# Performance work log

Hardware: AMD Instinct MI355X
Metric: run time of the kernel (lower is better)

The kernel has to match this reference:

```python
import jax, jax.numpy as jnp
import numpy as np

DIM = 1024
HIDDEN = 4096
NUM_EXPERTS = 8
TOP_K = 2
T = 8192


def setup_inputs() -> dict:
    key = jax.random.key(0)
    ks = jax.random.split(key, 5)
    scale = 0.02
    x = jax.random.normal(ks[0], (T, DIM), dtype=jnp.float32)
    gate_w = jax.random.normal(ks[1], (NUM_EXPERTS, DIM), dtype=jnp.float32) * scale  # Linear weight [out,in]
    w1 = jax.random.normal(ks[2], (NUM_EXPERTS, HIDDEN, DIM), dtype=jnp.float32) * scale
    w2 = jax.random.normal(ks[3], (NUM_EXPERTS, DIM, HIDDEN), dtype=jnp.float32) * scale
    w3 = jax.random.normal(ks[4], (NUM_EXPERTS, HIDDEN, DIM), dtype=jnp.float32) * scale
    return {"x": x, "gate_w": gate_w, "w1": w1, "w2": w2, "w3": w3}


def reference(x, gate_w, w1, w2, w3):
    # Router: softmax over all experts, take top-2, renormalize.
    logits = jnp.einsum('td,ed->te', x, gate_w)            # [T, E]
    probs = jax.nn.softmax(logits, axis=-1)
    topw, topi = jax.lax.top_k(probs, TOP_K)               # [T, 2]
    topw = topw / jnp.sum(topw, axis=-1, keepdims=True)
    out = jnp.zeros_like(x)
    num_experts = w1.shape[0]
    for e in range(num_experts):
        # combine weight for expert e per token (0 if not routed here)
        w_e = jnp.sum(jnp.where(topi == e, topw, 0.0), axis=-1)   # [T]
        h = jax.nn.silu(x @ w1[e].T) * (x @ w3[e].T)              # [T, HIDDEN]
        out = out + w_e[:, None] * (h @ w2[e].T)                  # [T, DIM]
    return out
```

## Files before the change

kernel.cpp:

```cpp
#include <hip/hip_runtime.h>
#include <hip/hip_bf16.h>
#include <cstdint>
#include <cstddef>

#define TK 8192
#define DIM 1024
#define HID 4096
#define NE 8

#define BMT 256
#define BNT 256
#define BKT 32
#define NBUF 4

typedef __attribute__((ext_vector_type(8))) __bf16 bfrag;
typedef __attribute__((ext_vector_type(4))) float ffrag;

static __device__ __forceinline__ ushort f2bf(float f) {
    union { float f; uint32_t u; } v; v.f = f;
    uint32_t r = (v.u + 0x7fffu + ((v.u >> 16) & 1u)) >> 16;
    return (ushort)r;
}

static __device__ __forceinline__ uint4 pack8(float4 a, float4 b) {
    union { ushort u[8]; uint4 q; } pk;
    pk.u[0] = f2bf(a.x); pk.u[1] = f2bf(a.y); pk.u[2] = f2bf(a.z); pk.u[3] = f2bf(a.w);
    pk.u[4] = f2bf(b.x); pk.u[5] = f2bf(b.y); pk.u[6] = f2bf(b.z); pk.u[7] = f2bf(b.w);
    return pk.q;
}

static __device__ __forceinline__ void gld16(const ushort* g, ushort* l) {
    __builtin_amdgcn_global_load_lds(
        (const __attribute__((address_space(1))) unsigned int*)g,
        (__attribute__((address_space(3))) unsigned int*)l, 16, 0, 0);
}

#define BARRIER() asm volatile("s_barrier" ::: "memory")
#define WAITVM(N) asm volatile("s_waitcnt vmcnt(" #N ")" ::: "memory")

#define LDSIDX(r, kc) ((((r) >> 3) << 8) + ((kc) << 6) + (((r) & 7) << 3))
#define SLOT_R(s)  ((((s) >> 5) << 3) | ((s) & 7))
#define SLOT_KC(s) (((s) >> 3) & 3)

__global__ __launch_bounds__(256) void k_cvt(const float* __restrict__ src,
                                             ushort* __restrict__ dst, int n8) {
    int i = blockIdx.x * blockDim.x + threadIdx.x;
    if (i >= n8) return;
    const float4* p = (const float4*)src + (size_t)i * 2;
    ((uint4*)dst)[i] = pack8(p[0], p[1]);
}

__global__ __launch_bounds__(256) void k_router(const float* __restrict__ x,
                                                const float* __restrict__ gw,
                                                int* __restrict__ topi, float* __restrict__ topw) {
    int t = blockIdx.x * 4 + (threadIdx.x >> 6);
    int lane = threadIdx.x & 63;
    if (t >= TK) return;
    double acc[NE];
#pragma unroll
    for (int e = 0; e < NE; ++e) acc[e] = 0.0;
    const float* xr = x + (size_t)t * DIM;
    for (int k = lane; k < DIM; k += 64) {
        double xv = (double)xr[k];
#pragma unroll
        for (int e = 0; e < NE; ++e) acc[e] += xv * (double)gw[e * DIM + k];
    }
#pragma unroll
    for (int e = 0; e < NE; ++e) {
#pragma unroll
        for (int off = 32; off > 0; off >>= 1) acc[e] += __shfl_xor(acc[e], off);
    }
    if (lane == 0) {
        int i1 = 0;
#pragma unroll
        for (int e = 1; e < NE; ++e) if (acc[e] > acc[i1]) i1 = e;
        int i2 = (i1 == 0) ? 1 : 0;
#pragma unroll
        for (int e = 0; e < NE; ++e) if (e != i1 && acc[e] > acc[i2]) i2 = e;
        double w = 1.0 / (1.0 + exp(acc[i2] - acc[i1]));
        topi[t * 2 + 0] = i1; topi[t * 2 + 1] = i2;
        topw[t * 2 + 0] = (float)w; topw[t * 2 + 1] = (float)(1.0 - w);
    }
}

__global__ void k_count(const int* __restrict__ topi, int* __restrict__ counts) {
    int i = blockIdx.x * blockDim.x + threadIdx.x;
    if (i < 2 * TK) atomicAdd(&counts[topi[i]], 1);
}

__global__ void k_scan(const int* __restrict__ counts, int* __restrict__ offs, int* __restrict__ cursor) {
    if (threadIdx.x == 0 && blockIdx.x == 0) {
        int s = 0;
        for (int e = 0; e < NE; ++e) { offs[e] = s; cursor[e] = s; s += counts[e]; }
        offs[NE] = s;
    }
}

__global__ void k_scatter(const int* __restrict__ topi, const float* __restrict__ topw,
                          int* __restrict__ cursor, int* __restrict__ perm, float* __restrict__ pw) {
    int t = blockIdx.x * blockDim.x + threadIdx.x;
    if (t >= TK) return;
#pragma unroll
    for (int k = 0; k < 2; ++k) {
        int e = topi[t * 2 + k];
        int pos = atomicAdd(&cursor[e], 1);
        perm[pos] = t; pw[pos] = topw[t * 2 + k];
    }
}

__global__ __launch_bounds__(512, 2) void k_ffn1(const ushort* __restrict__ xb,
                                                 const ushort* __restrict__ w1b,
                                                 const ushort* __restrict__ w3b,
                                                 const int* __restrict__ offs,
                                                 const int* __restrict__ perm,
                                                 ushort* __restrict__ H) {
    const int g = blockIdx.x;
    const int xcd = g & 7, kk = g >> 3;
    const int p  = xcd + ((kk >> 5) << 3);
    const int mt = kk & 31;
    const int e  = p >> 5, nt = p & 31;

    const int off = offs[e], end = offs[e + 1];
    const int m0 = off + mt * BMT;
    if (m0 >= end) return;
    const int nrows = min(BMT, end - m0);

    __shared__ ushort lA[NBUF][BMT * BKT];
    __shared__ ushort lB[NBUF][BNT * BKT];
    __shared__ int lTok[BMT];

    const int tid = threadIdx.x;
    if (tid < BMT) lTok[tid] = (tid < nrows) ? perm[m0 + tid] : -1;
    __syncthreads();

    const int lane = tid & 63, wid = tid >> 6;
    const int wm = (wid >> 2) * 128;
    const int wn = (wid & 3) * 64;

    ffrag acc[8][4];
#pragma unroll
    for (int i = 0; i < 8; ++i)
#pragma unroll
        for (int j = 0; j < 4; ++j) acc[i][j] = (ffrag)0.f;

    const ushort* pA[2]; const ushort* pB[2];
    {
        const size_t ebase = (size_t)e * HID * DIM;
#pragma unroll
        for (int i = 0; i < 2; ++i) {
            int s = i * 512 + tid;
            int r = SLOT_R(s), kc = SLOT_KC(s);
            int tok = lTok[r]; if (tok < 0) tok = 0;
            pA[i] = xb + (size_t)tok * DIM + kc * 8;
            int gg = r >> 4;
            int h  = ((gg >> 1) << 4) | (r & 15);
            const ushort* wsrc = (gg & 1) ? w3b : w1b;
            pB[i] = wsrc + ebase + (size_t)(nt * 128 + h) * DIM + kc * 8;
        }
    }

#define STG1A(buf, k0) do { \
        gld16(pA[0] + (k0), &lA[buf][(wid * 64) * 8]); \
        gld16(pA[1] + (k0), &lA[buf][(512 + wid * 64) * 8]); } while (0)
#define STG1B(buf, k0) do { \
        gld16(pB[0] + (k0), &lB[buf][(wid * 64) * 8]); \
        gld16(pB[1] + (k0), &lB[buf][(512 + wid * 64) * 8]); } while (0)

    STG1A(0, 0);  STG1B(0, 0);
    STG1A(1, 32); STG1B(1, 32);
    STG1A(2, 64); STG1B(2, 64);

    const int NT = DIM / BKT;
#pragma unroll 1
    for (int t = 0; t < NT; ++t) {
        const int cbuf = t & 3, sbuf = (t + 3) & 3;
        const bool stg = (t + 3) < NT;
        const int sk0 = (t + 3) * BKT;
        if (t + 2 < NT) { WAITVM(8); } else if (t + 1 < NT) { WAITVM(4); } else { WAITVM(0); }
        BARRIER();
        if (stg) STG1A(sbuf, sk0);
        const int kcc = lane >> 4;
        bfrag a[8], b[4];
#pragma unroll
        for (int j = 0; j < 4; ++j)
            b[j] = *(const bfrag*)&lB[cbuf][LDSIDX(wn + j * 16 + (lane & 15), kcc)];
#pragma unroll
        for (int i = 0; i < 4; ++i)
            a[i] = *(const bfrag*)&lA[cbuf][LDSIDX(wm + i * 16 + (lane & 15), kcc)];
        __builtin_amdgcn_s_setprio(1);
#pragma unroll
        for (int i = 0; i < 4; ++i)
#pragma unroll
            for (int j = 0; j < 4; ++j)
                acc[i][j] = __builtin_amdgcn_mfma_f32_16x16x32_bf16(a[i], b[j], acc[i][j], 0, 0, 0);
        __builtin_amdgcn_s_setprio(0);
        if (stg) STG1B(sbuf, sk0);
#pragma unroll
        for (int i = 4; i < 8; ++i)
            a[i] = *(const bfrag*)&lA[cbuf][LDSIDX(wm + i * 16 + (lane & 15), kcc)];
        __builtin_amdgcn_s_setprio(1);
#pragma unroll
        for (int i = 4; i < 8; ++i)
#pragma unroll
            for (int j = 0; j < 4; ++j)
                acc[i][j] = __builtin_amdgcn_mfma_f32_16x16x32_bf16(a[i], b[j], acc[i][j], 0, 0, 0);
        __builtin_amdgcn_s_setprio(0);
    }
#undef STG1A
#undef STG1B

#pragma unroll
    for (int i = 0; i < 8; ++i) {
        int rbase = wm + i * 16 + ((lane >> 4) << 2);
#pragma unroll
        for (int q = 0; q < 4; ++q) {
            int rl = rbase + q;
            if (rl >= nrows) continue;
            size_t rowoff = (size_t)(m0 + rl) * HID;
#pragma unroll
            for (int jf = 0; jf < 4; jf += 2) {
                int gg = (wn >> 4) + jf;
                int col = nt * 128 + ((gg >> 1) << 4) + (lane & 15);
                float h1 = acc[i][jf][q], h3 = acc[i][jf + 1][q];
                float val = (h1 / (1.f + __expf(-h1))) * h3;
                H[rowoff + col] = f2bf(val);
            }
        }
    }
}

__global__ __launch_bounds__(512, 2) void k_ffn2(const ushort* __restrict__ H,
                                                 const ushort* __restrict__ w2b,
                                                 const int* __restrict__ offs,
                                                 const int* __restrict__ perm,
                                                 const float* __restrict__ pw,
                                                 float* __restrict__ out) {
    const int g = blockIdx.x;
    const int xcd = g & 7, kk = g >> 3;
    const int p  = xcd + ((kk >> 5) << 3);
    const int mt = kk & 31;
    const int e  = p >> 2, nt = p & 3;

    const int off = offs[e], end = offs[e + 1];
    const int m0 = off + mt * BMT;
    if (m0 >= end) return;
    const int nrows = min(BMT, end - m0);

    __shared__ ushort lA[NBUF][BMT * BKT];
    __shared__ ushort lB[NBUF][BNT * BKT];
    __shared__ int lTok[BMT];
    __shared__ float lPw[BMT];

    const int tid = threadIdx.x;
    if (tid < BMT) {
        bool v = tid < nrows;
        lTok[tid] = v ? perm[m0 + tid] : -1;
        lPw[tid]  = v ? pw[m0 + tid] : 0.f;
    }
    __syncthreads();

    const int lane = tid & 63, wid = tid >> 6;
    const int wm = (wid >> 2) * 128;
    const int wn = (wid & 3) * 64;

    ffrag acc[8][4];
#pragma unroll
    for (int i = 0; i < 8; ++i)
#pragma unroll
        for (int j = 0; j < 4; ++j) acc[i][j] = (ffrag)0.f;

    const ushort* pA[2]; const ushort* pB[2];
    {
        const size_t ebase = (size_t)e * DIM * HID;
#pragma unroll
        for (int i = 0; i < 2; ++i) {
            int s = i * 512 + tid;
            int r = SLOT_R(s), kc = SLOT_KC(s);
            int pos = m0 + r; if (pos > 2 * TK - 1) pos = 2 * TK - 1;
            pA[i] = H + (size_t)pos * HID + kc * 8;
            pB[i] = w2b + ebase + (size_t)(nt * BNT + r) * HID + kc * 8;
        }
    }

#define STG2A(buf, k0) do { \
        gld16(pA[0] + (k0), &lA[buf][(wid * 64) * 8]); \
        gld16(pA[1] + (k0), &lA[buf][(512 + wid * 64) * 8]); } while (0)
#define STG2B(buf, k0) do { \
        gld16(pB[0] + (k0), &lB[buf][(wid * 64) * 8]); \
        gld16(pB[1] + (k0), &lB[buf][(512 + wid * 64) * 8]); } while (0)

    STG2A(0, 0);  STG2B(0, 0);
    STG2A(1, 32); STG2B(1, 32);
    STG2A(2, 64); STG2B(2, 64);

    const int NT = HID / BKT;
#pragma unroll 1
    for (int t = 0; t < NT; ++t) {
        const int cbuf = t & 3, sbuf = (t + 3) & 3;
        const bool stg = (t + 3) < NT;
        const int sk0 = (t + 3) * BKT;
        if (t + 2 < NT) { WAITVM(8); } else if (t + 1 < NT) { WAITVM(4); } else { WAITVM(0); }
        BARRIER();
        if (stg) STG2A(sbuf, sk0);
        const int kcc = lane >> 4;
        bfrag a[8], b[4];
#pragma unroll
        for (int j = 0; j < 4; ++j)
            b[j] = *(const bfrag*)&lB[cbuf][LDSIDX(wn + j * 16 + (lane & 15), kcc)];
#pragma unroll
        for (int i = 0; i < 4; ++i)
            a[i] = *(const bfrag*)&lA[cbuf][LDSIDX(wm + i * 16 + (lane & 15), kcc)];
        __builtin_amdgcn_s_setprio(1);
#pragma unroll
        for (int i = 0; i < 4; ++i)
#pragma unroll
            for (int j = 0; j < 4; ++j)
                acc[i][j] = __builtin_amdgcn_mfma_f32_16x16x32_bf16(a[i], b[j], acc[i][j], 0, 0, 0);
        __builtin_amdgcn_s_setprio(0);
        if (stg) STG2B(sbuf, sk0);
#pragma unroll
        for (int i = 4; i < 8; ++i)
            a[i] = *(const bfrag*)&lA[cbuf][LDSIDX(wm + i * 16 + (lane & 15), kcc)];
        __builtin_amdgcn_s_setprio(1);
#pragma unroll
        for (int i = 4; i < 8; ++i)
#pragma unroll
            for (int j = 0; j < 4; ++j)
                acc[i][j] = __builtin_amdgcn_mfma_f32_16x16x32_bf16(a[i], b[j], acc[i][j], 0, 0, 0);
        __builtin_amdgcn_s_setprio(0);
    }
#undef STG2A
#undef STG2B

    const int colbase = nt * BNT + wn;
#pragma unroll
    for (int i = 0; i < 8; ++i) {
        int rbase = wm + i * 16 + ((lane >> 4) << 2);
#pragma unroll
        for (int q = 0; q < 4; ++q) {
            int rl = rbase + q;
            if (rl >= nrows) continue;
            int tok = lTok[rl];
            float w = lPw[rl];
            if (tok < 0) continue;
            size_t rowoff = (size_t)tok * DIM;
#pragma unroll
            for (int j = 0; j < 4; ++j) {
                int col = colbase + j * 16 + (lane & 15);
                atomicAdd(&out[rowoff + col], acc[i][j][q] * w);
            }
        }
    }
}

extern "C" void kernel_launch(void* const* d_in, const int* in_sizes, int n_in,
                              void* d_out, int out_size, void* d_ws, size_t ws_size,
                              hipStream_t stream) {
    const float* x  = (const float*)d_in[0];
    const float* gw = (const float*)d_in[1];
    const float* w1 = (const float*)d_in[2];
    const float* w2 = (const float*)d_in[3];
    const float* w3 = (const float*)d_in[4];
    float* out = (float*)d_out;

    char* ws = (char*)d_ws;
    int*    topi   = (int*)(ws + 0);
    float*  topw   = (float*)(ws + 65536);
    int*    perm   = (int*)(ws + 131072);
    float*  pw     = (float*)(ws + 196608);
    int*    counts = (int*)(ws + 262144);
    int*    offs   = (int*)(ws + 262144 + 256);
    int*    cursor = (int*)(ws + 262144 + 512);

    const size_t OFF_XB = 524288;
    const size_t OFF_H  = OFF_XB + 16777216;
    const size_t OFF_WA = OFF_H + 134217728;
    const size_t OFF_WB = OFF_WA + 67108864;

    ushort* xb  = (ushort*)(ws + OFF_XB);
    ushort* H   = (ushort*)(ws + OFF_H);
    ushort* wA  = (ushort*)(ws + OFF_WA);
    ushort* wB  = (ushort*)(ws + OFF_WB);

    hipMemsetAsync(counts, 0, 32, stream);
    hipMemsetAsync(out, 0, (size_t)out_size * sizeof(float), stream);

    k_router<<<dim3(TK / 4), 256, 0, stream>>>(x, gw, topi, topw);
    k_count<<<dim3((2 * TK) / 256), 256, 0, stream>>>(topi, counts);
    k_scan<<<dim3(1), 64, 0, stream>>>(counts, offs, cursor);
    k_scatter<<<dim3(TK / 256), 256, 0, stream>>>(topi, topw, cursor, perm, pw);

    k_cvt<<<dim3((TK * DIM / 8) / 256), 256, 0, stream>>>(x, xb, TK * DIM / 8);
    k_cvt<<<dim3((NE * HID * DIM / 8) / 256), 256, 0, stream>>>(w1, wA, NE * HID * DIM / 8);
    k_cvt<<<dim3((NE * HID * DIM / 8) / 256), 256, 0, stream>>>(w3, wB, NE * HID * DIM / 8);

    k_ffn1<<<dim3(8192), 512, 0, stream>>>(xb, wA, wB, offs, perm, H);

    k_cvt<<<dim3((NE * DIM * HID / 8) / 256), 256, 0, stream>>>(w2, wA, NE * DIM * HID / 8);

    k_ffn2<<<dim3(1024), 512, 0, stream>>>(H, wA, offs, perm, pw, out);
}
```

Baseline: 1.202 ms.

## Restructure GEMM main loops into unrolled half-tile phases and regroup FFN2 block mapping

Both FFN GEMM loops are rewritten as a manually unrolled sequence of eight phases per four K-steps. Each phase loads half the A fragments, issues one stage of global-to-LDS prefetch, waits and barriers, then runs 16 MFMAs, in a ping-pong style schedule that keeps fewer A fragments in registers. In k_ffn2 the block-index mapping is changed so the four N-tiles of one M-tile land together on the same XCD, which should improve L2 reuse of the H rows. The extra barriers per phase add synchronization overhead and the waitcnt logic becomes less precise, which risks stalls or correctness issues near the end of the loop.

```diff
diff --git a/kernel.cpp b/kernel.cpp
--- a/kernel.cpp
+++ b/kernel.cpp
@@ -10,7 +10,7 @@
 
 #define BMT 256
 #define BNT 256
-#define BKT 32
+#define SK 32
 #define NBUF 4
 
 typedef __attribute__((ext_vector_type(8))) __bf16 bfrag;
@@ -107,6 +107,7 @@
         perm[pos] = t; pw[pos] = topw[t * 2 + k];
     }
 }
+
 
 __global__ __launch_bounds__(512, 2) void k_ffn1(const ushort* __restrict__ xb,
                                                  const ushort* __restrict__ w1b,
@@ -125,8 +126,8 @@
     if (m0 >= end) return;
     const int nrows = min(BMT, end - m0);
 
-    __shared__ ushort lA[NBUF][BMT * BKT];
-    __shared__ ushort lB[NBUF][BNT * BKT];
+    __shared__ ushort lA[NBUF][BMT * SK];
+    __shared__ ushort lB[NBUF][BNT * SK];
     __shared__ int lTok[BMT];
 
     const int tid = threadIdx.x;
@@ -134,6 +135,7 @@
     __syncthreads();
 
     const int lane = tid & 63, wid = tid >> 6;
+    const int l15 = lane & 15;
     const int wm = (wid >> 2) * 128;
     const int wn = (wid & 3) * 64;
 
@@ -159,55 +161,60 @@
         }
     }
 
-#define STG1A(buf, k0) do { \
-        gld16(pA[0] + (k0), &lA[buf][(wid * 64) * 8]); \
-        gld16(pA[1] + (k0), &lA[buf][(512 + wid * 64) * 8]); } while (0)
-#define STG1B(buf, k0) do { \
-        gld16(pB[0] + (k0), &lB[buf][(wid * 64) * 8]); \
-        gld16(pB[1] + (k0), &lB[buf][(512 + wid * 64) * 8]); } while (0)
-
-    STG1A(0, 0);  STG1B(0, 0);
-    STG1A(1, 32); STG1B(1, 32);
-    STG1A(2, 64); STG1B(2, 64);
-
-    const int NT = DIM / BKT;
+    const int NSUB = DIM / SK;
+
+#define STGA(buf, sx) do { if ((sx) < NSUB) { \
+        gld16(pA[0] + (sx) * SK, &lA[buf][(wid * 64) * 8]); \
+        gld16(pA[1] + (sx) * SK, &lA[buf][(512 + wid * 64) * 8]); } } while (0)
+#define STGB(buf, sx) do { if ((sx) < NSUB) { \
+        gld16(pB[0] + (sx) * SK, &lB[buf][(wid * 64) * 8]); \
+        gld16(pB[1] + (sx) * SK, &lB[buf][(512 + wid * 64) * 8]); } } while (0)
+
+    bfrag a[4], b[4];
+#define PH(buf, IH, STG) do {                                                   \
+        const int kcc = lane >> 4;                                              \
+        if (IH == 0) {                                                          \
+            _Pragma("unroll")                                                   \
+            for (int j = 0; j < 4; ++j)                                         \
+                b[j] = *(const bfrag*)&lB[buf][LDSIDX(wn + j * 16 + l15, kcc)]; \
+        }                                                                       \
+        _Pragma("unroll")                                                       \
+        for (int i = 0; i < 4; ++i)                                             \
+            a[i] = *(const bfrag*)&lA[buf][LDSIDX(wm + IH * 64 + i * 16 + l15, kcc)]; \
+        STG;                                                                    \
+        WAITVM(8); BARRIER();                                                   \
+        __builtin_amdgcn_s_setprio(1);                                          \
+        _Pragma("unroll")                                                       \
+        for (int i = 0; i < 4; ++i)                                             \
+            _Pragma("unroll")                                                   \
+            for (int j = 0; j < 4; ++j)                                         \
+                acc[IH * 4 + i][j] = __builtin_amdgcn_mfma_f32_16x16x32_bf16(a[i], b[j], acc[IH * 4 + i][j], 0, 0, 0); \
+        __builtin_amdgcn_s_setprio(0);                                          \
+        BARRIER();                                                              \
+    } while (0)
+
+    STGA(0, 0); STGB(0, 0);
+    STGA(1, 1); STGB(1, 1);
+    STGA(2, 2); STGB(2, 2);
+    WAITVM(8);
+    BARRIER();
+
 #pragma unroll 1
-    for (int t = 0; t < NT; ++t) {
-        const int cbuf = t & 3, sbuf = (t + 3) & 3;
-        const bool stg = (t + 3) < NT;
-        const int sk0 = (t + 3) * BKT;
-        if (t + 2 < NT) { WAITVM(8); } else if (t + 1 < NT) { WAITVM(4); } else { WAITVM(0); }
-        BARRIER();
-        if (stg) STG1A(sbuf, sk0);
-        const int kcc = lane >> 4;
-        bfrag a[8], b[4];
-#pragma unroll
-        for (int j = 0; j < 4; ++j)
-            b[j] = *(const bfrag*)&lB[cbuf][LDSIDX(wn + j * 16 + (lane & 15), kcc)];
-#pragma unroll
-        for (int i = 0; i < 4; ++i)
-            a[i] = *(const bfrag*)&lA[cbuf][LDSIDX(wm + i * 16 + (lane & 15), kcc)];
-        __builtin_amdgcn_s_setprio(1);
-#pragma unroll
-        for (int i = 0; i < 4; ++i)
-#pragma unroll
-            for (int j = 0; j < 4; ++j)
-                acc[i][j] = __builtin_amdgcn_mfma_f32_16x16x32_bf16(a[i], b[j], acc[i][j], 0, 0, 0);
-        __builtin_amdgcn_s_setprio(0);
-        if (stg) STG1B(sbuf, sk0);
-#pragma unroll
-        for (int i = 4; i < 8; ++i)
-            a[i] = *(const bfrag*)&lA[cbuf][LDSIDX(wm + i * 16 + (lane & 15), kcc)];
-        __builtin_amdgcn_s_setprio(1);
-#pragma unroll
-        for (int i = 4; i < 8; ++i)
-#pragma unroll
-            for (int j = 0; j < 4; ++j)
-                acc[i][j] = __builtin_amdgcn_mfma_f32_16x16x32_bf16(a[i], b[j], acc[i][j], 0, 0, 0);
-        __builtin_amdgcn_s_setprio(0);
-    }
-#undef STG1A
-#undef STG1B
+    for (int m = 0; m < NSUB / 4; ++m) {
+        const int s3 = 4 * m + 3, s4 = 4 * m + 4, s5 = 4 * m + 5, s6 = 4 * m + 6;
+        PH(0, 0, STGA(3, s3));
+        PH(0, 1, STGB(3, s3));
+        PH(1, 0, STGA(0, s4));
+        PH(1, 1, STGB(0, s4));
+        PH(2, 0, STGA(1, s5));
+        PH(2, 1, STGB(1, s5));
+        PH(3, 0, STGA(2, s6));
+        PH(3, 1, STGB(2, s6));
+    }
+    WAITVM(0);
+#undef PH
+#undef STGA
+#undef STGB
 
 #pragma unroll
     for (int i = 0; i < 8; ++i) {
@@ -220,7 +227,7 @@
 #pragma unroll
             for (int jf = 0; jf < 4; jf += 2) {
                 int gg = (wn >> 4) + jf;
-                int col = nt * 128 + ((gg >> 1) << 4) + (lane & 15);
+                int col = nt * 128 + ((gg >> 1) << 4) + l15;
                 float h1 = acc[i][jf][q], h3 = acc[i][jf + 1][q];
                 float val = (h1 / (1.f + __expf(-h1))) * h3;
                 H[rowoff + col] = f2bf(val);
@@ -236,18 +243,18 @@
                                                  const float* __restrict__ pw,
                                                  float* __restrict__ out) {
     const int g = blockIdx.x;
-    const int xcd = g & 7, kk = g >> 3;
-    const int p  = xcd + ((kk >> 5) << 3);
-    const int mt = kk & 31;
-    const int e  = p >> 2, nt = p & 3;
+    const int xcd = g & 7, k = g >> 3;
+    const int gg = xcd + ((k >> 2) << 3);
+    const int nt = k & 3;
+    const int e = gg >> 5, mt = gg & 31;
 
     const int off = offs[e], end = offs[e + 1];
     const int m0 = off + mt * BMT;
     if (m0 >= end) return;
     const int nrows = min(BMT, end - m0);
 
-    __shared__ ushort lA[NBUF][BMT * BKT];
-    __shared__ ushort lB[NBUF][BNT * BKT];
+    __shared__ ushort lA[NBUF][BMT * SK];
+    __shared__ ushort lB[NBUF][BNT * SK];
     __shared__ int lTok[BMT];
     __shared__ float lPw[BMT];
 
@@ -260,6 +267,7 @@
     __syncthreads();
 
     const int lane = tid & 63, wid = tid >> 6;
+    const int l15 = lane & 15;
     const int wm = (wid >> 2) * 128;
     const int wn = (wid & 3) * 64;
 
@@ -282,55 +290,60 @@
         }
     }
 
-#define STG2A(buf, k0) do { \
-        gld16(pA[0] + (k0), &lA[buf][(wid * 64) * 8]); \
-        gld16(pA[1] + (k0), &lA[buf][(512 + wid * 64) * 8]); } while (0)
-#define STG2B(buf, k0) do { \
-        gld16(pB[0] + (k0), &lB[buf][(wid * 64) * 8]); \
-        gld16(pB[1] + (k0), &lB[buf][(512 + wid * 64) * 8]); } while (0)
-
-    STG2A(0, 0);  STG2B(0, 0);
-    STG2A(1, 32); STG2B(1, 32);
-    STG2A(2, 64); STG2B(2, 64);
-
-    const int NT = HID / BKT;
+    const int NSUB = HID / SK;
+
+#define STGA(buf, sx) do { if ((sx) < NSUB) { \
+        gld16(pA[0] + (sx) * SK, &lA[buf][(wid * 64) * 8]); \
+        gld16(pA[1] + (sx) * SK, &lA[buf][(512 + wid * 64) * 8]); } } while (0)
+#define STGB(buf, sx) do { if ((sx) < NSUB) { \
+        gld16(pB[0] + (sx) * SK, &lB[buf][(wid * 64) * 8]); \
+        gld16(pB[1] + (sx) * SK, &lB[buf][(512 + wid * 64) * 8]); } } while (0)
+
+    bfrag a[4], b[4];
+#define PH(buf, IH, STG) do {                                                   \
+        const int kcc = lane >> 4;                                              \
+        if (IH == 0) {                                                          \
+            _Pragma("unroll")                                                   \
+            for (int j = 0; j < 4; ++j)                                         \
+                b[j] = *(const bfrag*)&lB[buf][LDSIDX(wn + j * 16 + l15, kcc)]; \
+        }                                                                       \
+        _Pragma("unroll")                                                       \
+        for (int i = 0; i < 4; ++i)                                             \
+            a[i] = *(const bfrag*)&lA[buf][LDSIDX(wm + IH * 64 + i * 16 + l15, kcc)]; \
+        STG;                                                                    \
+        WAITVM(8); BARRIER();                                                   \
+        __builtin_amdgcn_s_setprio(1);                                          \
+        _Pragma("unroll")                                                       \
+        for (int i = 0; i < 4; ++i)                                             \
+            _Pragma("unroll")                                                   \
+            for (int j = 0; j < 4; ++j)                                         \
+                acc[IH * 4 + i][j] = __builtin_amdgcn_mfma_f32_16x16x32_bf16(a[i], b[j], acc[IH * 4 + i][j], 0, 0, 0); \
+        __builtin_amdgcn_s_setprio(0);                                          \
+        BARRIER();                                                              \
+    } while (0)
+
+    STGA(0, 0); STGB(0, 0);
+    STGA(1, 1); STGB(1, 1);
+    STGA(2, 2); STGB(2, 2);
+    WAITVM(8);
+    BARRIER();
+
 #pragma unroll 1
-    for (int t = 0; t < NT; ++t) {
-        const int cbuf = t & 3, sbuf = (t + 3) & 3;
-        const bool stg = (t + 3) < NT;
-        const int sk0 = (t + 3) * BKT;
-        if (t + 2 < NT) { WAITVM(8); } else if (t + 1 < NT) { WAITVM(4); } else { WAITVM(0); }
-        BARRIER();
-        if (stg) STG2A(sbuf, sk0);
-        const int kcc = lane >> 4;
-        bfrag a[8], b[4];
-#pragma unroll
-        for (int j = 0; j < 4; ++j)
-            b[j] = *(const bfrag*)&lB[cbuf][LDSIDX(wn + j * 16 + (lane & 15), kcc)];
-#pragma unroll
-        for (int i = 0; i < 4; ++i)
-            a[i] = *(const bfrag*)&lA[cbuf][LDSIDX(wm + i * 16 + (lane & 15), kcc)];
-        __builtin_amdgcn_s_setprio(1);
-#pragma unroll
-        for (int i = 0; i < 4; ++i)
-#pragma unroll
-            for (int j = 0; j < 4; ++j)
-                acc[i][j] = __builtin_amdgcn_mfma_f32_16x16x32_bf16(a[i], b[j], acc[i][j], 0, 0, 0);
-        __builtin_amdgcn_s_setprio(0);
-        if (stg) STG2B(sbuf, sk0);
-#pragma unroll
-        for (int i = 4; i < 8; ++i)
-            a[i] = *(const bfrag*)&lA[cbuf][LDSIDX(wm + i * 16 + (lane & 15), kcc)];
-        __builtin_amdgcn_s_setprio(1);
-#pragma unroll
-        for (int i = 4; i < 8; ++i)
-#pragma unroll
-            for (int j = 0; j < 4; ++j)
-                acc[i][j] = __builtin_amdgcn_mfma_f32_16x16x32_bf16(a[i], b[j], acc[i][j], 0, 0, 0);
-        __builtin_amdgcn_s_setprio(0);
-    }
-#undef STG2A
-#undef STG2B
+    for (int m = 0; m < NSUB / 4; ++m) {
+        const int s3 = 4 * m + 3, s4 = 4 * m + 4, s5 = 4 * m + 5, s6 = 4 * m + 6;
+        PH(0, 0, STGA(3, s3));
+        PH(0, 1, STGB(3, s3));
+        PH(1, 0, STGA(0, s4));
+        PH(1, 1, STGB(0, s4));
+        PH(2, 0, STGA(1, s5));
+        PH(2, 1, STGB(1, s5));
+        PH(3, 0, STGA(2, s6));
+        PH(3, 1, STGB(2, s6));
+    }
+    WAITVM(0);
+#undef PH
+#undef STGA
+#undef STGB
 
     const int colbase = nt * BNT + wn;
 #pragma unroll
@@ -346,7 +359,7 @@
             size_t rowoff = (size_t)tok * DIM;
 #pragma unroll
             for (int j = 0; j < 4; ++j) {
-                int col = colbase + j * 16 + (lane & 15);
+                int col = colbase + j * 16 + l15;
                 atomicAdd(&out[rowoff + col], acc[i][j][q] * w);
             }
         }
```

New measurement: 1.021 ms. 15.1% less time.

## Persistent grouped-GEMM kernels with compact tile descriptors and smaller M tiles

Applied to the files above, without the earlier changes.

The scan kernel now builds a compact list of (expert, m-tile) descriptors, and both FFN kernels become persistent grid-stride loops over only the valid work items. Before, most of the 8192 launched blocks exited early. M tiles shrink from 256 to 128 rows, the pipeline drops from 4 buffers to 3, and launch bounds rise to 4 blocks per CU to raise occupancy and cut the padding waste from partial tiles. In exchange, each 128-row tile now reloads its full weight slice, so total weight traffic doubles, and the XCD-aware block remapping is gone, which may hurt L2 locality.

```diff
diff --git a/kernel.cpp b/kernel.cpp
--- a/kernel.cpp
+++ b/kernel.cpp
@@ -8,10 +8,11 @@
 #define HID 4096
 #define NE 8
 
-#define BMT 256
-#define BNT 256
-#define BKT 32
-#define NBUF 4
+#define SK 32
+#define NSUB1 (DIM / SK)
+#define NSUB2 (HID / SK)
+#define ASZ (512 * 8)
+#define BSZ (1024 * 8)
 
 typedef __attribute__((ext_vector_type(8))) __bf16 bfrag;
 typedef __attribute__((ext_vector_type(4))) float ffrag;
@@ -88,11 +89,19 @@
     if (i < 2 * TK) atomicAdd(&counts[topi[i]], 1);
 }
 
-__global__ void k_scan(const int* __restrict__ counts, int* __restrict__ offs, int* __restrict__ cursor) {
+__global__ void k_scan(const int* __restrict__ counts, int* __restrict__ offs,
+                       int* __restrict__ cursor, int* __restrict__ desc,
+                       int* __restrict__ ndesc) {
     if (threadIdx.x == 0 && blockIdx.x == 0) {
-        int s = 0;
-        for (int e = 0; e < NE; ++e) { offs[e] = s; cursor[e] = s; s += counts[e]; }
+        int s = 0, d = 0;
+        for (int e = 0; e < NE; ++e) {
+            offs[e] = s; cursor[e] = s;
+            int tiles = (counts[e] + 127) >> 7;
+            for (int t = 0; t < tiles; ++t) desc[d++] = (e << 16) | t;
+            s += counts[e];
+        }
         offs[NE] = s;
+        ndesc[0] = d;
     }
 }
 
@@ -108,246 +117,251 @@
     }
 }
 
-__global__ __launch_bounds__(512, 2) void k_ffn1(const ushort* __restrict__ xb,
+
+__global__ __launch_bounds__(512, 4) void k_ffn1(const ushort* __restrict__ xb,
                                                  const ushort* __restrict__ w1b,
                                                  const ushort* __restrict__ w3b,
                                                  const int* __restrict__ offs,
                                                  const int* __restrict__ perm,
+                                                 const int* __restrict__ desc,
+                                                 const int* __restrict__ ndesc_g,
                                                  ushort* __restrict__ H) {
-    const int g = blockIdx.x;
-    const int xcd = g & 7, kk = g >> 3;
-    const int p  = xcd + ((kk >> 5) << 3);
-    const int mt = kk & 31;
-    const int e  = p >> 5, nt = p & 31;
-
-    const int off = offs[e], end = offs[e + 1];
-    const int m0 = off + mt * BMT;
-    if (m0 >= end) return;
-    const int nrows = min(BMT, end - m0);
-
-    __shared__ ushort lA[NBUF][BMT * BKT];
-    __shared__ ushort lB[NBUF][BNT * BKT];
-    __shared__ int lTok[BMT];
+    __shared__ ushort lA[3 * ASZ];
+    __shared__ ushort lB[3 * BSZ];
+    __shared__ int lTok[128];
 
     const int tid = threadIdx.x;
-    if (tid < BMT) lTok[tid] = (tid < nrows) ? perm[m0 + tid] : -1;
-    __syncthreads();
-
     const int lane = tid & 63, wid = tid >> 6;
-    const int wm = (wid >> 2) * 128;
+    const int l15 = lane & 15, kcc = lane >> 4;
+    const int wm = (wid >> 2) * 64;
     const int wn = (wid & 3) * 64;
 
-    ffrag acc[8][4];
-#pragma unroll
-    for (int i = 0; i < 8; ++i)
-#pragma unroll
-        for (int j = 0; j < 4; ++j) acc[i][j] = (ffrag)0.f;
-
-    const ushort* pA[2]; const ushort* pB[2];
-    {
-        const size_t ebase = (size_t)e * HID * DIM;
-#pragma unroll
-        for (int i = 0; i < 2; ++i) {
-            int s = i * 512 + tid;
-            int r = SLOT_R(s), kc = SLOT_KC(s);
-            int tok = lTok[r]; if (tok < 0) tok = 0;
-            pA[i] = xb + (size_t)tok * DIM + kc * 8;
-            int gg = r >> 4;
-            int h  = ((gg >> 1) << 4) | (r & 15);
-            const ushort* wsrc = (gg & 1) ? w3b : w1b;
-            pB[i] = wsrc + ebase + (size_t)(nt * 128 + h) * DIM + kc * 8;
-        }
-    }
-
-#define STG1A(buf, k0) do { \
-        gld16(pA[0] + (k0), &lA[buf][(wid * 64) * 8]); \
-        gld16(pA[1] + (k0), &lA[buf][(512 + wid * 64) * 8]); } while (0)
-#define STG1B(buf, k0) do { \
-        gld16(pB[0] + (k0), &lB[buf][(wid * 64) * 8]); \
-        gld16(pB[1] + (k0), &lB[buf][(512 + wid * 64) * 8]); } while (0)
-
-    STG1A(0, 0);  STG1B(0, 0);
-    STG1A(1, 32); STG1B(1, 32);
-    STG1A(2, 64); STG1B(2, 64);
-
-    const int NT = DIM / BKT;
+    const int nitems = ndesc_g[0] << 5;
+
+    const int rA = SLOT_R(tid), kcA = SLOT_KC(tid);
+
+    bfrag a[4], b[4];
+    ffrag acc[4][4];
+
 #pragma unroll 1
-    for (int t = 0; t < NT; ++t) {
-        const int cbuf = t & 3, sbuf = (t + 3) & 3;
-        const bool stg = (t + 3) < NT;
-        const int sk0 = (t + 3) * BKT;
-        if (t + 2 < NT) { WAITVM(8); } else if (t + 1 < NT) { WAITVM(4); } else { WAITVM(0); }
-        BARRIER();
-        if (stg) STG1A(sbuf, sk0);
-        const int kcc = lane >> 4;
-        bfrag a[8], b[4];
-#pragma unroll
-        for (int j = 0; j < 4; ++j)
-            b[j] = *(const bfrag*)&lB[cbuf][LDSIDX(wn + j * 16 + (lane & 15), kcc)];
+    for (int w = blockIdx.x; w < nitems; w += (int)gridDim.x) {
+        __syncthreads();
+        const int de = desc[w >> 5];
+        const int e = de >> 16, mt = de & 0xffff, nt = w & 31;
+        const int m0 = offs[e] + (mt << 7);
+        const int nrows = min(128, offs[e + 1] - m0);
+        if (tid < 128) lTok[tid] = (tid < nrows) ? perm[m0 + tid] : perm[m0];
+        __syncthreads();
+
+        const ushort* pA = xb + (size_t)lTok[rA] * DIM + kcA * 8;
+        const ushort* pBp[2];
+        {
+            const size_t ebase = (size_t)e * HID * DIM;
+#pragma unroll
+            for (int i2 = 0; i2 < 2; ++i2) {
+                int s = i2 * 512 + tid;
+                int r = SLOT_R(s), kc = SLOT_KC(s);
+                int gg = r >> 4;
+                int h = ((gg >> 1) << 4) | (r & 15);
+                const ushort* wsrc = (gg & 1) ? w3b : w1b;
+                pBp[i2] = wsrc + ebase + (size_t)(nt * 128 + h) * DIM + kc * 8;
+            }
+        }
+
 #pragma unroll
         for (int i = 0; i < 4; ++i)
-            a[i] = *(const bfrag*)&lA[cbuf][LDSIDX(wm + i * 16 + (lane & 15), kcc)];
-        __builtin_amdgcn_s_setprio(1);
-#pragma unroll
-        for (int i = 0; i < 4; ++i)
-#pragma unroll
-            for (int j = 0; j < 4; ++j)
-                acc[i][j] = __builtin_amdgcn_mfma_f32_16x16x32_bf16(a[i], b[j], acc[i][j], 0, 0, 0);
-        __builtin_amdgcn_s_setprio(0);
-        if (stg) STG1B(sbuf, sk0);
-#pragma unroll
-        for (int i = 4; i < 8; ++i)
-            a[i] = *(const bfrag*)&lA[cbuf][LDSIDX(wm + i * 16 + (lane & 15), kcc)];
-        __builtin_amdgcn_s_setprio(1);
-#pragma unroll
-        for (int i = 4; i < 8; ++i)
-#pragma unroll
-            for (int j = 0; j < 4; ++j)
-                acc[i][j] = __builtin_amdgcn_mfma_f32_16x16x32_bf16(a[i], b[j], acc[i][j], 0, 0, 0);
-        __builtin_amdgcn_s_setprio(0);
-    }
-#undef STG1A
-#undef STG1B
-
-#pragma unroll
-    for (int i = 0; i < 8; ++i) {
-        int rbase = wm + i * 16 + ((lane >> 4) << 2);
-#pragma unroll
-        for (int q = 0; q < 4; ++q) {
-            int rl = rbase + q;
-            if (rl >= nrows) continue;
-            size_t rowoff = (size_t)(m0 + rl) * HID;
-#pragma unroll
-            for (int jf = 0; jf < 4; jf += 2) {
-                int gg = (wn >> 4) + jf;
-                int col = nt * 128 + ((gg >> 1) << 4) + (lane & 15);
-                float h1 = acc[i][jf][q], h3 = acc[i][jf + 1][q];
-                float val = (h1 / (1.f + __expf(-h1))) * h3;
-                H[rowoff + col] = f2bf(val);
+#pragma unroll
+            for (int j = 0; j < 4; ++j) acc[i][j] = (ffrag)0.f;
+
+#define STG1(buf, sx) do { if ((sx) < NSUB1) {                                   \
+            gld16(pA + (sx) * SK, lA + (buf) * ASZ + (wid * 64) * 8);            \
+            gld16(pBp[0] + (sx) * SK, lB + (buf) * BSZ + (wid * 64) * 8);        \
+            gld16(pBp[1] + (sx) * SK, lB + (buf) * BSZ + (512 + wid * 64) * 8); } } while (0)
+
+        STG1(0, 0);
+        STG1(1, 1);
+        int bc = 0, bs = 2;
+#pragma unroll 1
+        for (int X = 0; X < NSUB1 - 1; ++X) {
+            WAITVM(3);
+            BARRIER();
+            const ushort* A_ = lA + bc * ASZ;
+            const ushort* B_ = lB + bc * BSZ;
+#pragma unroll
+            for (int j = 0; j < 4; ++j) b[j] = *(const bfrag*)&B_[LDSIDX(wn + j * 16 + l15, kcc)];
+#pragma unroll
+            for (int i = 0; i < 4; ++i) a[i] = *(const bfrag*)&A_[LDSIDX(wm + i * 16 + l15, kcc)];
+            STG1(bs, X + 2);
+            __builtin_amdgcn_s_setprio(1);
+#pragma unroll
+            for (int i = 0; i < 4; ++i)
+#pragma unroll
+                for (int j = 0; j < 4; ++j)
+                    acc[i][j] = __builtin_amdgcn_mfma_f32_16x16x32_bf16(a[i], b[j], acc[i][j], 0, 0, 0);
+            __builtin_amdgcn_s_setprio(0);
+            bc = (bc == 2) ? 0 : bc + 1;
+            bs = (bs == 2) ? 0 : bs + 1;
+        }
+        {
+            WAITVM(0);
+            BARRIER();
+            const ushort* A_ = lA + bc * ASZ;
+            const ushort* B_ = lB + bc * BSZ;
+#pragma unroll
+            for (int j = 0; j < 4; ++j) b[j] = *(const bfrag*)&B_[LDSIDX(wn + j * 16 + l15, kcc)];
+#pragma unroll
+            for (int i = 0; i < 4; ++i) a[i] = *(const bfrag*)&A_[LDSIDX(wm + i * 16 + l15, kcc)];
+            __builtin_amdgcn_s_setprio(1);
+#pragma unroll
+            for (int i = 0; i < 4; ++i)
+#pragma unroll
+                for (int j = 0; j < 4; ++j)
+                    acc[i][j] = __builtin_amdgcn_mfma_f32_16x16x32_bf16(a[i], b[j], acc[i][j], 0, 0, 0);
+            __builtin_amdgcn_s_setprio(0);
+        }
+#undef STG1
+
+#pragma unroll
+        for (int i = 0; i < 4; ++i) {
+            int rbase = wm + i * 16 + ((lane >> 4) << 2);
+#pragma unroll
+            for (int q = 0; q < 4; ++q) {
+                int rl = rbase + q;
+                if (rl >= nrows) continue;
+                size_t rowoff = (size_t)(m0 + rl) * HID;
+#pragma unroll
+                for (int jf = 0; jf < 4; jf += 2) {
+                    int gg = (wn >> 4) + jf;
+                    int col = nt * 128 + ((gg >> 1) << 4) + l15;
+                    float h1 = acc[i][jf][q], h3 = acc[i][jf + 1][q];
+                    H[rowoff + col] = f2bf((h1 / (1.f + __expf(-h1))) * h3);
+                }
             }
         }
     }
 }
 
-__global__ __launch_bounds__(512, 2) void k_ffn2(const ushort* __restrict__ H,
+__global__ __launch_bounds__(512, 4) void k_ffn2(const ushort* __restrict__ H,
                                                  const ushort* __restrict__ w2b,
                                                  const int* __restrict__ offs,
                                                  const int* __restrict__ perm,
                                                  const float* __restrict__ pw,
+                                                 const int* __restrict__ desc,
+                                                 const int* __restrict__ ndesc_g,
                                                  float* __restrict__ out) {
-    const int g = blockIdx.x;
-    const int xcd = g & 7, kk = g >> 3;
-    const int p  = xcd + ((kk >> 5) << 3);
-    const int mt = kk & 31;
-    const int e  = p >> 2, nt = p & 3;
-
-    const int off = offs[e], end = offs[e + 1];
-    const int m0 = off + mt * BMT;
-    if (m0 >= end) return;
-    const int nrows = min(BMT, end - m0);
-
-    __shared__ ushort lA[NBUF][BMT * BKT];
-    __shared__ ushort lB[NBUF][BNT * BKT];
-    __shared__ int lTok[BMT];
-    __shared__ float lPw[BMT];
+    __shared__ ushort lA[3 * ASZ];
+    __shared__ ushort lB[3 * BSZ];
+    __shared__ int lTok[128];
+    __shared__ float lPw[128];
 
     const int tid = threadIdx.x;
-    if (tid < BMT) {
-        bool v = tid < nrows;
-        lTok[tid] = v ? perm[m0 + tid] : -1;
-        lPw[tid]  = v ? pw[m0 + tid] : 0.f;
-    }
-    __syncthreads();
-
     const int lane = tid & 63, wid = tid >> 6;
-    const int wm = (wid >> 2) * 128;
+    const int l15 = lane & 15, kcc = lane >> 4;
+    const int wm = (wid >> 2) * 64;
     const int wn = (wid & 3) * 64;
 
-    ffrag acc[8][4];
-#pragma unroll
-    for (int i = 0; i < 8; ++i)
-#pragma unroll
-        for (int j = 0; j < 4; ++j) acc[i][j] = (ffrag)0.f;
-
-    const ushort* pA[2]; const ushort* pB[2];
-    {
-        const size_t ebase = (size_t)e * DIM * HID;
-#pragma unroll
-        for (int i = 0; i < 2; ++i) {
-            int s = i * 512 + tid;
-            int r = SLOT_R(s), kc = SLOT_KC(s);
-            int pos = m0 + r; if (pos > 2 * TK - 1) pos = 2 * TK - 1;
-            pA[i] = H + (size_t)pos * HID + kc * 8;
-            pB[i] = w2b + ebase + (size_t)(nt * BNT + r) * HID + kc * 8;
-        }
-    }
-
-#define STG2A(buf, k0) do { \
-        gld16(pA[0] + (k0), &lA[buf][(wid * 64) * 8]); \
-        gld16(pA[1] + (k0), &lA[buf][(512 + wid * 64) * 8]); } while (0)
-#define STG2B(buf, k0) do { \
-        gld16(pB[0] + (k0), &lB[buf][(wid * 64) * 8]); \
-        gld16(pB[1] + (k0), &lB[buf][(512 + wid * 64) * 8]); } while (0)
-
-    STG2A(0, 0);  STG2B(0, 0);
-    STG2A(1, 32); STG2B(1, 32);
-    STG2A(2, 64); STG2B(2, 64);
-
-    const int NT = HID / BKT;
+    const int nitems = ndesc_g[0] << 2;
+
+    const int rA = SLOT_R(tid), kcA = SLOT_KC(tid);
+
+    bfrag a[4], b[4];
+    ffrag acc[4][4];
+
 #pragma unroll 1
-    for (int t = 0; t < NT; ++t) {
-        const int cbuf = t & 3, sbuf = (t + 3) & 3;
-        const bool stg = (t + 3) < NT;
-        const int sk0 = (t + 3) * BKT;
-        if (t + 2 < NT) { WAITVM(8); } else if (t + 1 < NT) { WAITVM(4); } else { WAITVM(0); }
-        BARRIER();
-        if (stg) STG2A(sbuf, sk0);
-        const int kcc = lane >> 4;
-        bfrag a[8], b[4];
-#pragma unroll
-        for (int j = 0; j < 4; ++j)
-            b[j] = *(const bfrag*)&lB[cbuf][LDSIDX(wn + j * 16 + (lane & 15), kcc)];
+    for (int w = blockIdx.x; w < nitems; w += (int)gridDim.x) {
+        __syncthreads();
+        const int de = desc[w >> 2];
+        const int e = de >> 16, mt = de & 0xffff, nt = w & 3;
+        const int m0 = offs[e] + (mt << 7);
+        const int nrows = min(128, offs[e + 1] - m0);
+        if (tid < 128) {
+            bool v = tid < nrows;
+            lTok[tid] = v ? perm[m0 + tid] : 0;
+            lPw[tid]  = v ? pw[m0 + tid] : 0.f;
+        }
+        __syncthreads();
+
+        int posA = m0 + rA; if (posA > 2 * TK - 1) posA = 2 * TK - 1;
+        const ushort* pA = H + (size_t)posA * HID + kcA * 8;
+        const ushort* pBp[2];
+        {
+            const size_t ebase = (size_t)e * DIM * HID;
+#pragma unroll
+            for (int i2 = 0; i2 < 2; ++i2) {
+                int s = i2 * 512 + tid;
+                int r = SLOT_R(s), kc = SLOT_KC(s);
+                pBp[i2] = w2b + ebase + (size_t)(nt * 256 + r) * HID + kc * 8;
+            }
+        }
+
 #pragma unroll
         for (int i = 0; i < 4; ++i)
-            a[i] = *(const bfrag*)&lA[cbuf][LDSIDX(wm + i * 16 + (lane & 15), kcc)];
-        __builtin_amdgcn_s_setprio(1);
-#pragma unroll
-        for (int i = 0; i < 4; ++i)
-#pragma unroll
-            for (int j = 0; j < 4; ++j)
-                acc[i][j] = __builtin_amdgcn_mfma_f32_16x16x32_bf16(a[i], b[j], acc[i][j], 0, 0, 0);
-        __builtin_amdgcn_s_setprio(0);
-        if (stg) STG2B(sbuf, sk0);
-#pragma unroll
-        for (int i = 4; i < 8; ++i)
-            a[i] = *(const bfrag*)&lA[cbuf][LDSIDX(wm + i * 16 + (lane & 15), kcc)];
-        __builtin_amdgcn_s_setprio(1);
-#pragma unroll
-        for (int i = 4; i < 8; ++i)
-#pragma unroll
-            for (int j = 0; j < 4; ++j)
-                acc[i][j] = __builtin_amdgcn_mfma_f32_16x16x32_bf16(a[i], b[j], acc[i][j], 0, 0, 0);
-        __builtin_amdgcn_s_setprio(0);
-    }
-#undef STG2A
-#undef STG2B
-
-    const int colbase = nt * BNT + wn;
-#pragma unroll
-    for (int i = 0; i < 8; ++i) {
-        int rbase = wm + i * 16 + ((lane >> 4) << 2);
-#pragma unroll
-        for (int q = 0; q < 4; ++q) {
-            int rl = rbase + q;
-            if (rl >= nrows) continue;
-            int tok = lTok[rl];
-            float w = lPw[rl];
-            if (tok < 0) continue;
-            size_t rowoff = (size_t)tok * DIM;
-#pragma unroll
-            for (int j = 0; j < 4; ++j) {
-                int col = colbase + j * 16 + (lane & 15);
-                atomicAdd(&out[rowoff + col], acc[i][j][q] * w);
+#pragma unroll
+            for (int j = 0; j < 4; ++j) acc[i][j] = (ffrag)0.f;
+
+#define STG2(buf, sx) do { if ((sx) < NSUB2) {                                   \
+            gld16(pA + (sx) * SK, lA + (buf) * ASZ + (wid * 64) * 8);            \
+            gld16(pBp[0] + (sx) * SK, lB + (buf) * BSZ + (wid * 64) * 8);        \
+            gld16(pBp[1] + (sx) * SK, lB + (buf) * BSZ + (512 + wid * 64) * 8); } } while (0)
+
+        STG2(0, 0);
+        STG2(1, 1);
+        int bc = 0, bs = 2;
+#pragma unroll 1
+        for (int X = 0; X < NSUB2 - 1; ++X) {
+            WAITVM(3);
+            BARRIER();
+            const ushort* A_ = lA + bc * ASZ;
+            const ushort* B_ = lB + bc * BSZ;
+#pragma unroll
+            for (int j = 0; j < 4; ++j) b[j] = *(const bfrag*)&B_[LDSIDX(wn + j * 16 + l15, kcc)];
+#pragma unroll
+            for (int i = 0; i < 4; ++i) a[i] = *(const bfrag*)&A_[LDSIDX(wm + i * 16 + l15, kcc)];
+            STG2(bs, X + 2);
+            __builtin_amdgcn_s_setprio(1);
+#pragma unroll
+            for (int i = 0; i < 4; ++i)
+#pragma unroll
+                for (int j = 0; j < 4; ++j)
+                    acc[i][j] = __builtin_amdgcn_mfma_f32_16x16x32_bf16(a[i], b[j], acc[i][j], 0, 0, 0);
+            __builtin_amdgcn_s_setprio(0);
+            bc = (bc == 2) ? 0 : bc + 1;
+            bs = (bs == 2) ? 0 : bs + 1;
+        }
+        {
+            WAITVM(0);
+            BARRIER();
+            const ushort* A_ = lA + bc * ASZ;
+            const ushort* B_ = lB + bc * BSZ;
+#pragma unroll
+            for (int j = 0; j < 4; ++j) b[j] = *(const bfrag*)&B_[LDSIDX(wn + j * 16 + l15, kcc)];
+#pragma unroll
+            for (int i = 0; i < 4; ++i) a[i] = *(const bfrag*)&A_[LDSIDX(wm + i * 16 + l15, kcc)];
+            __builtin_amdgcn_s_setprio(1);
+#pragma unroll
+            for (int i = 0; i < 4; ++i)
+#pragma unroll
+                for (int j = 0; j < 4; ++j)
+                    acc[i][j] = __builtin_amdgcn_mfma_f32_16x16x32_bf16(a[i], b[j], acc[i][j], 0, 0, 0);
+            __builtin_amdgcn_s_setprio(0);
+        }
+#undef STG2
+
+#pragma unroll
+        for (int i = 0; i < 4; ++i) {
+            int rbase = wm + i * 16 + ((lane >> 4) << 2);
+#pragma unroll
+            for (int q = 0; q < 4; ++q) {
+                int rl = rbase + q;
+                if (rl >= nrows) continue;
+                int tok = lTok[rl];
+                float wgt = lPw[rl];
+                size_t rowoff = (size_t)tok * DIM;
+#pragma unroll
+                for (int j = 0; j < 4; ++j) {
+                    int col = nt * 256 + wn + j * 16 + l15;
+                    atomicAdd(&out[rowoff + col], acc[i][j][q] * wgt);
+                }
             }
         }
     }
@@ -371,6 +385,8 @@
     int*    counts = (int*)(ws + 262144);
     int*    offs   = (int*)(ws + 262144 + 256);
     int*    cursor = (int*)(ws + 262144 + 512);
+    int*    ndesc  = (int*)(ws + 262144 + 768);
+    int*    desc   = (int*)(ws + 262144 + 1024);
 
     const size_t OFF_XB = 524288;
     const size_t OFF_H  = OFF_XB + 16777216;
@@ -387,16 +403,16 @@
 
     k_router<<<dim3(TK / 4), 256, 0, stream>>>(x, gw, topi, topw);
     k_count<<<dim3((2 * TK) / 256), 256, 0, stream>>>(topi, counts);
-    k_scan<<<dim3(1), 64, 0, stream>>>(counts, offs, cursor);
+    k_scan<<<dim3(1), 64, 0, stream>>>(counts, offs, cursor, desc, ndesc);
     k_scatter<<<dim3(TK / 256), 256, 0, stream>>>(topi, topw, cursor, perm, pw);
 
     k_cvt<<<dim3((TK * DIM / 8) / 256), 256, 0, stream>>>(x, xb, TK * DIM / 8);
     k_cvt<<<dim3((NE * HID * DIM / 8) / 256), 256, 0, stream>>>(w1, wA, NE * HID * DIM / 8);
     k_cvt<<<dim3((NE * HID * DIM / 8) / 256), 256, 0, stream>>>(w3, wB, NE * HID * DIM / 8);
 
-    k_ffn1<<<dim3(8192), 512, 0, stream>>>(xb, wA, wB, offs, perm, H);
+    k_ffn1<<<dim3(512), 512, 0, stream>>>(xb, wA, wB, offs, perm, desc, ndesc, H);
 
     k_cvt<<<dim3((NE * DIM * HID / 8) / 256), 256, 0, stream>>>(w2, wA, NE * DIM * HID / 8);
 
-    k_ffn2<<<dim3(1024), 512, 0, stream>>>(H, wA, offs, perm, pw, out);
-}
+    k_ffn2<<<dim3(512), 512, 0, stream>>>(H, wA, offs, perm, pw, desc, ndesc, out);
+}
```

New measurement: 1.003 ms. -16.6%, faster.
